# Kernel tuning notes

Hardware: AMD Instinct MI355X
Metric: run time of the kernel (lower is better)

## Reference

```python
import jax, jax.numpy as jnp
import numpy as np

WS = 32          # window_size (== k passed to rounding helper)
R = 4            # num_relations
H = 8            # num_heads
D = 64           # out_features (head dim)
FIN = 256        # in_features
LENGTHS = [251, 247, 263, 255, 240, 258, 249, 260, 252, 245, 256, 250, 248, 261, 244, 254]


def _statics(lengths, ws):
    """Static index bookkeeping mirroring round_up_to_nearest_k_and_a_window_size,
    insert_zero_rows and the post-hoc index removal in forward()."""
    l = np.asarray(lengths, dtype=np.int64)
    tgt = (l + ws - 1) // ws * ws + ws            # per-graph padded length (+1 extra window)
    starts = np.concatenate([[0], np.cumsum(tgt)[:-1]])
    pad_even = starts - np.arange(len(l)) * ws + l  # padding start in trimmed frame
    pad_odd_win = (starts + tgt - ws) // ws         # window index of each extra padding window
    L = int(tgt.sum())
    w = L // ws
    # positions of real nodes inside the padded sequence
    pos = np.concatenate([s + np.arange(n) for s, n in zip(starts, l)])
    extra = set(pad_odd_win.tolist())
    rem_windows = np.array([i for i in range(w) if i not in extra], dtype=np.int64)
    Wp = len(rem_windows)
    removed = set()
    for p in pad_even:
        nm = (int(p) + ws - 1) // ws * ws
        removed.update(range(int(p), nm))
    rem_final = np.array([i for i in range(Wp * ws) if i not in removed], dtype=np.int64)
    return L, w, pos, rem_windows, rem_final


def setup_inputs() -> dict:
    key = jax.random.key(0)
    k1, k2, k3, k4, k5 = jax.random.split(key, 5)
    N = int(sum(LENGTHS))
    node_features = jax.random.normal(k1, (R, N, FIN), dtype=jnp.float32)
    Wq = jax.random.normal(k2, (H * D, FIN), dtype=jnp.float32) * 0.02
    b_q = jax.random.normal(k3, (H * D,), dtype=jnp.float32) * 0.02
    Wk = jax.random.normal(k4, (H * D, FIN), dtype=jnp.float32) * 0.02
    b_k = jax.random.normal(k5, (H * D,), dtype=jnp.float32) * 0.02
    num_nodes = jnp.asarray(LENGTHS, dtype=jnp.int64)
    return {"node_features": node_features, "Wq": Wq, "b_q": b_q, "Wk": Wk, "b_k": b_k,
            "num_nodes": num_nodes}


def reference(node_features, Wq, b_q, Wk, b_k, num_nodes):
    lengths = np.asarray(num_nodes).tolist()
    L, w, pos, rem_w, rem_f = _statics(lengths, WS)
    Rr, N, Fi = node_features.shape

    # insert_zero_rows: scatter real nodes into padded [R, L, F]; bool key mask [L]
    padded = jnp.zeros((Rr, L, Fi), node_features.dtype).at[:, pos].set(node_features)
    maskL = np.zeros(L, dtype=bool)
    maskL[pos] = True

    # Q/K projections -> [R*H, L, D]
    Q = (padded @ Wq.T + b_q).reshape(Rr, L, H, D).transpose(0, 2, 1, 3).reshape(Rr * H, L, D)
    K = (padded @ Wk.T + b_k).reshape(Rr, L, H, D).transpose(0, 2, 1, 3).reshape(Rr * H, L, D)

    scale = D ** -0.5
    qb = Q.reshape(-1, w, WS, D) * scale            # [B, w, ws, D]
    kb = K.reshape(-1, w, WS, D)
    # look_around keys (backward=1, forward=1, pad_value=-1)
    pk = jnp.pad(kb, ((0, 0), (1, 1), (0, 0), (0, 0)), constant_values=-1.0)
    k3 = jnp.concatenate([pk[:, i:i + w] for i in range(3)], axis=2)  # [B, w, 3ws, D]

    # static validity mask: key-position pad mask AND look-around of real-node mask
    t = np.arange(L).reshape(w, WS)
    pt = np.pad(t, ((1, 1), (0, 0)), constant_values=-1)
    t3 = np.concatenate([pt[i:i + w] for i in range(3)], axis=1)      # [w, 3ws]
    mw = maskL.reshape(w, WS)
    pm = np.pad(mw, ((1, 1), (0, 0)), constant_values=False)
    m3 = np.concatenate([pm[i:i + w] for i in range(3)], axis=1)      # [w, 3ws]
    valid = jnp.asarray(m3 & (t3 != -1))[None, :, None, :]            # [1, w, 1, 3ws]

    sim = jnp.einsum('bwid,bwjd->bwij', qb, k3)                        # [B, w, ws, 3ws]
    NEG = -jnp.finfo(sim.dtype).max
    sim = jnp.where(valid, sim, NEG)

    # drop pure-padding extra windows, softmax (dropout omitted: eval mode)
    attn = jax.nn.softmax(sim[:, rem_w], axis=-1)                      # [B, Wp, ws, 3ws]
    Wp = rem_w.shape[0]
    score = attn.reshape(Rr, H, Wp, WS, 3 * WS).mean(axis=1)           # [R, Wp, ws, 3ws]

    # displace blocks to banded rectangle, then trim first/last window of columns
    wi = np.arange(Wp)[:, None, None]
    ri = np.arange(WS)[None, :, None]
    ci = (np.arange(Wp) * WS)[:, None, None] + np.arange(3 * WS)[None, None, :]
    full = jnp.zeros((Rr, Wp, WS, (Wp + 2) * WS), score.dtype)
    full = full.at[:, wi, ri, ci].set(score)
    rect = full.reshape(Rr, Wp * WS, (Wp + 2) * WS)[:, :, WS:-WS]      # [R, Wp*ws, Wp*ws]

    # remove intra-window padding rows and columns
    rect = rect[:, rem_f][:, :, rem_f]                                 # [R, N, N]
    n = rem_f.shape[0]
    return rect.transpose(1, 0, 2).reshape(n, Rr * n)                  # [N, R*N]
```

## Files before the change

kernel.cpp:

```cpp
#include <hip/hip_runtime.h>
#include <stdint.h>

typedef float f32x4 __attribute__((ext_vector_type(4)));
typedef short s16x8 __attribute__((ext_vector_type(8)));
typedef unsigned short u16x4 __attribute__((ext_vector_type(4)));
typedef unsigned short u16x8 __attribute__((ext_vector_type(8)));

#define NG 16
__constant__ int c_LEN[NG]   = {251,247,263,255,240,258,249,260,252,245,256,250,248,261,244,254};
__constant__ int c_CUM[NG+1] = {0,251,498,761,1016,1256,1514,1763,2023,2275,2520,2776,3026,3274,3535,3779,4033};
__constant__ int c_KWC[NG+1] = {0,8,16,25,33,41,50,58,67,75,83,91,99,107,116,124,132};

#define NTOT 4033
#define RN   16132
#define NWIN 132
#define NEGF (-3.0e38f)

#define OUT_N4  16265089L
#define PBLK   253
#define ZB     1795

#define OFF_QK 524288

__device__ __forceinline__ unsigned short f2bf(float f){
  union { float f; uint32_t u; } x; x.f = f;
  uint32_t u = x.u;
  u += 0x7fffu + ((u >> 16) & 1u);
  return (unsigned short)(u >> 16);
}

__device__ __forceinline__ f32x4 mfma16(s16x8 a, s16x8 b, f32x4 c){
  return __builtin_amdgcn_mfma_f32_16x16x32_bf16(a, b, c, 0, 0, 0);
}

#define WCH 65536
__global__ __launch_bounds__(256) void wcvt_kernel(const float* __restrict__ Wq,
                                                   const float* __restrict__ Wk,
                                                   unsigned short* __restrict__ Wb){
  for (int j = blockIdx.x * 256 + threadIdx.x; j < WCH; j += 64 * 256){
    const float* src = (j < WCH/2) ? (Wq + (size_t)j * 4)
                                   : (Wk + (size_t)(j - WCH/2) * 4);
    f32x4 v = *(const f32x4*)src;
    u16x4 o;
    #pragma unroll
    for (int c = 0; c < 4; ++c) o[c] = f2bf(v[c]);
    *(u16x4*)(Wb + (size_t)j * 4) = o;
  }
}

#define LP 68
__global__ __launch_bounds__(256) void projzero_kernel(const float* __restrict__ X,
                                                       const unsigned short* __restrict__ Wb,
                                                       const float* __restrict__ bq,
                                                       const float* __restrict__ bk,
                                                       unsigned short* __restrict__ QK,
                                                       float* __restrict__ out){
  __shared__ char smem[64 * 264 * 2];
  unsigned short* xs = (unsigned short*)smem;
  float* tile = (float*)smem;

  int bid = blockIdx.x;
  if (bid >= PBLK){
    int grp = bid - PBLK;
    f32x4 z = {0.f, 0.f, 0.f, 0.f};
    f32x4* o4 = (f32x4*)out;
    long stride = (long)ZB * 256;
    for (long i = (long)grp * 256 + threadIdx.x; i < OUT_N4; i += stride)
      __builtin_nontemporal_store(z, o4 + i);
    return;
  }

  int tid  = threadIdx.x;
  int row0 = bid * 64;

  for (int c = tid; c < 4096; c += 256){
    int rr = c >> 6, c4 = c & 63;
    int gr = min(row0 + rr, RN - 1);
    f32x4 v = *(const f32x4*)(X + (size_t)gr * 256 + c4 * 4);
    u16x4 o;
    #pragma unroll
    for (int i = 0; i < 4; ++i) o[i] = f2bf(v[i]);
    *(u16x4*)(xs + rr * 264 + c4 * 4) = o;
  }
  __syncthreads();

  int lane = tid & 63, wid = tid >> 6;
  int l15  = lane & 15, quad = lane >> 4;
  int wm = wid & 1, wn = wid >> 1;

  s16x8 aR[2][8];
  #pragma unroll
  for (int m = 0; m < 2; ++m)
    #pragma unroll
    for (int kk = 0; kk < 8; ++kk)
      aR[m][kk] = *(const s16x8*)(xs + (wm * 32 + m * 16 + l15) * 264 + kk * 32 + quad * 8);

  for (int ct = 0; ct < 16; ++ct){
    int col0 = ct * 64;
    int colW = col0 + wn * 32;
    const unsigned short* b0p = Wb + (size_t)(colW + l15)      * 256 + quad * 8;
    const unsigned short* b1p = Wb + (size_t)(colW + 16 + l15) * 256 + quad * 8;

    f32x4 acc[2][2];
    #pragma unroll
    for (int m = 0; m < 2; ++m)
      #pragma unroll
      for (int n = 0; n < 2; ++n){ acc[m][n][0]=0.f; acc[m][n][1]=0.f; acc[m][n][2]=0.f; acc[m][n][3]=0.f; }

    #pragma unroll
    for (int kk = 0; kk < 8; ++kk){
      s16x8 b0 = *(const s16x8*)(b0p + kk * 32);
      s16x8 b1 = *(const s16x8*)(b1p + kk * 32);
      acc[0][0] = mfma16(aR[0][kk], b0, acc[0][0]);
      acc[0][1] = mfma16(aR[0][kk], b1, acc[0][1]);
      acc[1][0] = mfma16(aR[1][kk], b0, acc[1][0]);
      acc[1][1] = mfma16(aR[1][kk], b1, acc[1][1]);
    }

    __syncthreads();
    #pragma unroll
    for (int m = 0; m < 2; ++m)
    #pragma unroll
    for (int n = 0; n < 2; ++n)
    #pragma unroll
    for (int g = 0; g < 4; ++g){
      int rL = wm * 32 + m * 16 + quad * 4 + g;
      int cL = wn * 32 + n * 16 + l15;
      tile[rL * LP + cL] = acc[m][n][g];
    }
    __syncthreads();

    int rL = tid >> 2;
    int cB = (tid & 3) * 16;
    int row = row0 + rL;
    if (row < RN){
      int col = col0 + cB;
      const float* bias = (col < 512) ? (bq + col) : (bk + col - 512);
      float sc = (col < 512) ? 0.125f : 1.0f;
      u16x8 o0, o1;
      #pragma unroll
      for (int i = 0; i < 8; ++i)
        o0[i] = f2bf((tile[rL * LP + cB + i] + bias[i]) * sc);
      #pragma unroll
      for (int i = 0; i < 8; ++i)
        o1[i] = f2bf((tile[rL * LP + cB + 8 + i] + bias[8 + i]) * sc);
      *(u16x8*)(QK + (size_t)row * 1024 + col)     = o0;
      *(u16x8*)(QK + (size_t)row * 1024 + col + 8) = o1;
    }
  }
}

__global__ __launch_bounds__(512) void attn_kernel(const unsigned short* __restrict__ QK,
                                                   float* __restrict__ out){
  __shared__ float part[4][32 * 97];

  int b  = blockIdx.x;
  int r  = b / NWIN;
  int wq = b % NWIN;
  int g = 0;
  #pragma unroll
  for (int i = 0; i < NG; ++i) if (wq >= c_KWC[i + 1]) g = i + 1;
  int lw   = wq - c_KWC[g];
  int l    = c_LEN[g];
  int base = c_CUM[g];
  int qbeg = lw * 32;
  int qnum = min(32, l - qbeg);
  int kbeg = max(0, qbeg - 32);
  int kend = min(l, qbeg + 64);
  int knum = kend - kbeg;

  int tid  = threadIdx.x;
  int lane = tid & 63, wid = tid >> 6;
  int l15  = lane & 15, quad = lane >> 4;
  int rbase = r * NTOT + base;
  int h = wid;

  bool valid[6];
  #pragma unroll
  for (int n = 0; n < 6; ++n) valid[n] = (n * 16 + l15) < knum;

  s16x8 qf[2][2];
  #pragma unroll
  for (int m = 0; m < 2; ++m){
    int qi = min(qbeg + m * 16 + l15, l - 1);
    const unsigned short* qp = QK + (size_t)(rbase + qi) * 1024 + h * 64 + quad * 8;
    qf[m][0] = *(const s16x8*)qp;
    qf[m][1] = *(const s16x8*)(qp + 32);
  }
  f32x4 s[2][6];
  #pragma unroll
  for (int n = 0; n < 6; ++n){
    int ki = min(kbeg + n * 16 + l15, l - 1);
    const unsigned short* kp = QK + (size_t)(rbase + ki) * 1024 + 512 + h * 64 + quad * 8;
    s16x8 kf0 = *(const s16x8*)kp;
    s16x8 kf1 = *(const s16x8*)(kp + 32);
    #pragma unroll
    for (int m = 0; m < 2; ++m){
      f32x4 z; z[0]=0.f; z[1]=0.f; z[2]=0.f; z[3]=0.f;
      z = mfma16(qf[m][0], kf0, z);
      s[m][n] = mfma16(qf[m][1], kf1, z);
    }
  }
  #pragma unroll
  for (int m = 0; m < 2; ++m)
    #pragma unroll
    for (int n = 0; n < 6; ++n)
      if (!valid[n]){ s[m][n][0]=NEGF; s[m][n][1]=NEGF; s[m][n][2]=NEGF; s[m][n][3]=NEGF; }

  #pragma unroll
  for (int m = 0; m < 2; ++m){
    f32x4 mx = s[m][0];
    #pragma unroll
    for (int n = 1; n < 6; ++n)
      #pragma unroll
      for (int c = 0; c < 4; ++c) mx[c] = fmaxf(mx[c], s[m][n][c]);
    #pragma unroll
    for (int c = 0; c < 4; ++c){
      float v = mx[c];
      v = fmaxf(v, __shfl_xor(v, 1));
      v = fmaxf(v, __shfl_xor(v, 2));
      v = fmaxf(v, __shfl_xor(v, 4));
      v = fmaxf(v, __shfl_xor(v, 8));
      mx[c] = v;
    }
    f32x4 sum; sum[0]=0.f; sum[1]=0.f; sum[2]=0.f; sum[3]=0.f;
    #pragma unroll
    for (int n = 0; n < 6; ++n)
      #pragma unroll
      for (int c = 0; c < 4; ++c){
        float e = __expf(s[m][n][c] - mx[c]);
        s[m][n][c] = e;
        sum[c] += e;
      }
    #pragma unroll
    for (int c = 0; c < 4; ++c){
      float v = sum[c];
      v += __shfl_xor(v, 1);
      v += __shfl_xor(v, 2);
      v += __shfl_xor(v, 4);
      v += __shfl_xor(v, 8);
      sum[c] = v;
    }
    f32x4 scv;
    #pragma unroll
    for (int c = 0; c < 4; ++c) scv[c] = 0.125f / sum[c];
    #pragma unroll
    for (int n = 0; n < 6; ++n)
      #pragma unroll
      for (int c = 0; c < 4; ++c) s[m][n][c] *= scv[c];
  }

  if (wid >= 4){
    #pragma unroll
    for (int m = 0; m < 2; ++m)
    #pragma unroll
    for (int n = 0; n < 6; ++n)
    #pragma unroll
    for (int c = 0; c < 4; ++c){
      int row = m * 16 + quad * 4 + c;
      int col = n * 16 + l15;
      part[wid - 4][row * 97 + col] = s[m][n][c];
    }
  }
  __syncthreads();
  if (wid < 4){
    #pragma unroll
    for (int m = 0; m < 2; ++m)
    #pragma unroll
    for (int n = 0; n < 6; ++n)
    #pragma unroll
    for (int c = 0; c < 4; ++c){
      int row = m * 16 + quad * 4 + c;
      int col = n * 16 + l15;
      part[wid][row * 97 + col] += s[m][n][c];
    }
  }
  __syncthreads();

  for (int e = tid; e < 32 * 96; e += 512){
    int row = e / 96, col = e % 96;
    if (row < qnum && col < knum){
      float v = part[0][row * 97 + col] + part[1][row * 97 + col]
              + part[2][row * 97 + col] + part[3][row * 97 + col];
      long nq = base + qbeg + row;
      long mk = base + kbeg + col;
      out[nq * (long)RN + (long)r * NTOT + mk] = v;
    }
  }
}

extern "C" void kernel_launch(void* const* d_in, const int* in_sizes, int n_in,
                              void* d_out, int out_size, void* d_ws, size_t ws_size,
                              hipStream_t stream){
  const float* X  = (const float*)d_in[0];
  const float* Wq = (const float*)d_in[1];
  const float* bq = (const float*)d_in[2];
  const float* Wk = (const float*)d_in[3];
  const float* bk = (const float*)d_in[4];
  float* out = (float*)d_out;

  char* ws = (char*)d_ws;
  unsigned short* Wb = (unsigned short*)ws;
  unsigned short* QK = (unsigned short*)(ws + OFF_QK);

  wcvt_kernel<<<64, 256, 0, stream>>>(Wq, Wk, Wb);
  projzero_kernel<<<PBLK + ZB, 256, 0, stream>>>(X, Wb, bq, bk, QK, out);
  attn_kernel<<<4 * NWIN, 512, 0, stream>>>(QK, out);
}
```

Before: 352.6 us.

## Fuse output zero-fill into attention kernel, skipping band regions

Removes the dedicated zero-fill blocks from the projection launch. Each attention block now zeroes its own query rows for one column slice of the output, skipping the banded columns that the attention results will overwrite. This avoids writing the band twice and places the large memset inside the attention launch. The cost is branchy per-element handling where a float4 straddles a relation boundary or a band edge, and the zero-fill no longer overlaps with the projection.

```diff
diff --git a/kernel.cpp b/kernel.cpp
--- a/kernel.cpp
+++ b/kernel.cpp
@@ -16,9 +16,7 @@
 #define NWIN 132
 #define NEGF (-3.0e38f)
 
-#define OUT_N4  16265089L
-#define PBLK   253
-#define ZB     1795
+#define PBLK 253
 
 #define OFF_QK 524288
 
@@ -49,29 +47,17 @@
 }
 
 #define LP 68
-__global__ __launch_bounds__(256) void projzero_kernel(const float* __restrict__ X,
-                                                       const unsigned short* __restrict__ Wb,
-                                                       const float* __restrict__ bq,
-                                                       const float* __restrict__ bk,
-                                                       unsigned short* __restrict__ QK,
-                                                       float* __restrict__ out){
+__global__ __launch_bounds__(256) void proj_kernel(const float* __restrict__ X,
+                                                   const unsigned short* __restrict__ Wb,
+                                                   const float* __restrict__ bq,
+                                                   const float* __restrict__ bk,
+                                                   unsigned short* __restrict__ QK){
   __shared__ char smem[64 * 264 * 2];
   unsigned short* xs = (unsigned short*)smem;
   float* tile = (float*)smem;
 
-  int bid = blockIdx.x;
-  if (bid >= PBLK){
-    int grp = bid - PBLK;
-    f32x4 z = {0.f, 0.f, 0.f, 0.f};
-    f32x4* o4 = (f32x4*)out;
-    long stride = (long)ZB * 256;
-    for (long i = (long)grp * 256 + threadIdx.x; i < OUT_N4; i += stride)
-      __builtin_nontemporal_store(z, o4 + i);
-    return;
-  }
-
   int tid  = threadIdx.x;
-  int row0 = bid * 64;
+  int row0 = blockIdx.x * 64;
 
   for (int c = tid; c < 4096; c += 256){
     int rr = c >> 6, c4 = c & 63;
@@ -168,12 +154,50 @@
   int kbeg = max(0, qbeg - 32);
   int kend = min(l, qbeg + 64);
   int knum = kend - kbeg;
+  int KB = base + kbeg;
+  int KE = base + kend;
 
   int tid  = threadIdx.x;
   int lane = tid & 63, wid = tid >> 6;
   int l15  = lane & 15, quad = lane >> 4;
   int rbase = r * NTOT + base;
   int h = wid;
+
+  {
+    int cs = r ? 1009 + 1008 * (r - 1) : 0;
+    int ce = 1009 + 1008 * r;
+    f32x4 z = {0.f, 0.f, 0.f, 0.f};
+    for (int rr = wid; rr < qnum; rr += 8){
+      float* orow = out + (size_t)(base + qbeg + rr) * RN;
+      for (int c = cs + lane; c < ce; c += 64){
+        int col0 = c << 2;
+        int r0 = (col0 >= 12099) ? 3 : (col0 >= 8066) ? 2 : (col0 >= 4033) ? 1 : 0;
+        int col3 = col0 + 3;
+        int r3 = (col3 >= 12099) ? 3 : (col3 >= 8066) ? 2 : (col3 >= 4033) ? 1 : 0;
+        if (r0 == r3){
+          int cr = col0 - r0 * NTOT;
+          if (cr + 4 <= KB || cr >= KE){
+            __builtin_nontemporal_store(z, (f32x4*)(orow + col0));
+          } else if (cr >= KB && cr + 4 <= KE){
+          } else {
+            #pragma unroll
+            for (int i = 0; i < 4; ++i){
+              int cc = cr + i;
+              if (cc < KB || cc >= KE) orow[col0 + i] = 0.f;
+            }
+          }
+        } else {
+          #pragma unroll
+          for (int i = 0; i < 4; ++i){
+            int col = col0 + i;
+            int rx = (col >= 12099) ? 3 : (col >= 8066) ? 2 : (col >= 4033) ? 1 : 0;
+            int cr = col - rx * NTOT;
+            if (cr < KB || cr >= KE) orow[col] = 0.f;
+          }
+        }
+      }
+    }
+  }
 
   bool valid[6];
   #pragma unroll
@@ -283,8 +307,7 @@
       float v = part[0][row * 97 + col] + part[1][row * 97 + col]
               + part[2][row * 97 + col] + part[3][row * 97 + col];
       long nq = base + qbeg + row;
-      long mk = base + kbeg + col;
-      out[nq * (long)RN + (long)r * NTOT + mk] = v;
+      out[nq * (long)RN + (long)r * NTOT + KB + col] = v;
     }
   }
 }
@@ -304,6 +327,6 @@
   unsigned short* QK = (unsigned short*)(ws + OFF_QK);
 
   wcvt_kernel<<<64, 256, 0, stream>>>(Wq, Wk, Wb);
-  projzero_kernel<<<PBLK + ZB, 256, 0, stream>>>(X, Wb, bq, bk, QK, out);
+  proj_kernel<<<PBLK, 256, 0, stream>>>(X, Wb, bq, bk, QK);
   attn_kernel<<<4 * NWIN, 512, 0, stream>>>(QK, out);
 }
```

Result: slower. 379.0 us (+7.5%).
